# Optimization experiments

Hardware: AMD Instinct MI355X
Metric: run time of the kernel (lower is better)

## Reference

```python
import jax, jax.numpy as jnp
import numpy as np

B, N, C_IN, H, C_OUT = 8, 1024, 256, 4, 256
C = C_OUT // H  # per-head dim = 64
ALPHA = 0.2
NEG_INF = -9e15


def setup_inputs() -> dict:
    key = jax.random.key(0)
    k1, k2, k3, k4, k5 = jax.random.split(key, 5)
    node_feats = jax.random.normal(k1, (B, N, C_IN), dtype=jnp.float32)
    adj_matrix = jax.random.randint(k2, (B, N, N), 0, 2, dtype=jnp.int32)
    # include self-loops as GAT expects
    eye = jnp.eye(N, dtype=jnp.int32)[None]
    adj_matrix = jnp.maximum(adj_matrix, eye)
    # xavier_uniform with gain=1.414
    def xavier(k, shape, fan_in, fan_out, gain=1.414):
        lim = gain * np.sqrt(6.0 / (fan_in + fan_out))
        return jax.random.uniform(k, shape, jnp.float32, -lim, lim)
    W = xavier(k3, (C_OUT, C_IN), C_IN, C_OUT)          # projection weight [out,in]
    b = jnp.zeros((C_OUT,), dtype=jnp.float32)           # projection bias
    a = xavier(k4, (H, 2 * C), 2 * C, H)                 # attention vector per head
    return {"node_feats": node_feats, "adj_matrix": adj_matrix, "W": W, "b": b, "a": a}


def reference(node_feats, adj_matrix, W, b, a):
    Bb, Nn, _ = node_feats.shape
    Hh, twoC = a.shape
    Cc = twoC // 2
    # linear projection -> [B, N, H, C]
    h = (node_feats @ W.T + b).reshape(Bb, Nn, Hh, Cc)
    # edge logit(i,j) = leakyrelu(a . [h_i, h_j]) = leakyrelu(a1.h_i + a2.h_j)
    a_src, a_dst = a[:, :Cc], a[:, Cc:]
    l_src = jnp.einsum('bihc,hc->bih', h, a_src)  # [B,N,H]
    l_dst = jnp.einsum('bjhc,hc->bjh', h, a_dst)  # [B,N,H]
    logits = jax.nn.leaky_relu(l_src[:, :, None, :] + l_dst[:, None, :, :], ALPHA)  # [B,N,N,H]
    logits = jnp.where(adj_matrix[..., None] == 1, logits, NEG_INF)
    probs = jax.nn.softmax(logits, axis=2)  # softmax over neighbors j
    out = jnp.einsum('bijh,bjhc->bihc', probs, h)  # aggregate
    return out.reshape(Bb, Nn, Hh * Cc)  # concat heads
```

## Files before the change

kernel.cpp:

```cpp
#include <hip/hip_runtime.h>
#include <hip/hip_bf16.h>

#define BN   8
#define NN   1024
#define CIN  256
#define COUT 256
#define HH   4
#define CC   64
#define ALPHA_C 0.2f

typedef __attribute__((ext_vector_type(8))) short short8;
typedef __attribute__((ext_vector_type(4))) float f32x4;

__device__ __forceinline__ unsigned short f2bf(float x) {
    __hip_bfloat16 h = __float2bfloat16(x);
    return *(unsigned short*)&h;
}
__device__ __forceinline__ float bf2f(unsigned short u) {
    return __uint_as_float(((unsigned int)u) << 16);
}

__global__ __launch_bounds__(256) void k0_wpack(
    const float* __restrict__ W, unsigned short* __restrict__ Whp, unsigned short* __restrict__ Wlp)
{
    const int bid = blockIdx.x;
    const int n = threadIdx.x;
    const int fi = n * 64 + (bid >> 2) * 8 + (bid & 3) * 2;
    const float4* W4 = (const float4*)W;
    float4 wa = W4[fi], wb = W4[fi + 1];
    float xs[8] = {wa.x, wa.y, wa.z, wa.w, wb.x, wb.y, wb.z, wb.w};
    unsigned short hh[8], ll[8];
    #pragma unroll
    for (int e = 0; e < 8; ++e) {
        hh[e] = f2bf(xs[e]);
        ll[e] = f2bf(xs[e] - bf2f(hh[e]));
    }
    *(uint4*)(Whp + ((size_t)bid * 256 + n) * 8) = *(uint4*)hh;
    *(uint4*)(Wlp + ((size_t)bid * 256 + n) * 8) = *(uint4*)ll;
}

__global__ __launch_bounds__(1024, 4) void k1_gemm(
    const float* __restrict__ X, const float* __restrict__ bias, const float* __restrict__ a,
    const unsigned short* __restrict__ Whp, const unsigned short* __restrict__ Wlp,
    unsigned short* __restrict__ hbf_p, float* __restrict__ lsrc_t, float* __restrict__ ldst_t)
{
    __shared__ __align__(16) unsigned short Xh[32 * 256];
    __shared__ __align__(16) unsigned short Xl[32 * 256];
    __shared__ float lsP[2][8][2][16];

    const int bid = blockIdx.x;
    const int row0 = bid * 32;
    const int b  = bid >> 5;
    const int tj = bid & 31;
    const int tid = threadIdx.x;
    const int wv = tid >> 6, l = tid & 63, il = l & 15, jg = l >> 4;
    const int mq = wv >> 3, no = wv & 7;

    {
        const float4* X4 = (const float4*)(X + (size_t)row0 * CIN);
        #pragma unroll
        for (int it = 0; it < 2; ++it) {
            int f = it * 1024 + tid;
            int r = f >> 6, k4 = f & 63;
            float4 x = X4[f];
            unsigned short h0 = f2bf(x.x), h1 = f2bf(x.y), h2 = f2bf(x.z), h3 = f2bf(x.w);
            unsigned short l0 = f2bf(x.x - bf2f(h0)), l1 = f2bf(x.y - bf2f(h1));
            unsigned short l2 = f2bf(x.z - bf2f(h2)), l3 = f2bf(x.w - bf2f(h3));
            unsigned short hs[4] = {h0, h1, h2, h3}, ls[4] = {l0, l1, l2, l3};
            int off = r * 512 + ((k4 * 8) ^ ((r & 7) << 4));
            *(uint2*)((char*)Xh + off) = *(uint2*)hs;
            *(uint2*)((char*)Xl + off) = *(uint2*)ls;
        }
    }
    __syncthreads();

    f32x4 acc0 = {0.f, 0.f, 0.f, 0.f}, acc1 = acc0;
    {
        const int abase = (mq * 16 + il) * 512;
        const int swz = (il & 7) << 4;
        const short8* Wh8 = (const short8*)Whp;
        const short8* Wl8 = (const short8*)Wlp;
        const int nb = no * 32 + il;
        #pragma unroll
        for (int kc = 0; kc < 8; ++kc) {
            const int ab = abase + ((kc * 64 + jg * 16) ^ swz);
            short8 Ah = *(const short8*)((const char*)Xh + ab);
            short8 Al = *(const short8*)((const char*)Xl + ab);
            const int pidx = (kc * 4 + jg) * 256 + nb;
            short8 Bh0 = Wh8[pidx],      Bl0 = Wl8[pidx];
            short8 Bh1 = Wh8[pidx + 16], Bl1 = Wl8[pidx + 16];
            acc0 = __builtin_amdgcn_mfma_f32_16x16x32_bf16(Ah, Bh0, acc0, 0, 0, 0);
            acc1 = __builtin_amdgcn_mfma_f32_16x16x32_bf16(Ah, Bh1, acc1, 0, 0, 0);
            acc0 = __builtin_amdgcn_mfma_f32_16x16x32_bf16(Ah, Bl0, acc0, 0, 0, 0);
            acc1 = __builtin_amdgcn_mfma_f32_16x16x32_bf16(Ah, Bl1, acc1, 0, 0, 0);
            acc0 = __builtin_amdgcn_mfma_f32_16x16x32_bf16(Al, Bh0, acc0, 0, 0, 0);
            acc1 = __builtin_amdgcn_mfma_f32_16x16x32_bf16(Al, Bh1, acc1, 0, 0, 0);
        }
    }

    const int c0 = no * 32 + il, c1 = c0 + 16;
    const float bia0 = bias[c0], bia1 = bias[c1];
    const int hh = no >> 1;
    const int cc0 = c0 & 63, cc1 = c1 & 63;
    const float as0 = a[hh * 128 + cc0],      as1 = a[hh * 128 + cc1];
    const float ad0 = a[hh * 128 + 64 + cc0], ad1 = a[hh * 128 + 64 + cc1];

    float v0[4], v1[4], psrc[4], pdst[4];
    #pragma unroll
    for (int r = 0; r < 4; ++r) {
        v0[r] = acc0[r] + bia0;
        v1[r] = acc1[r] + bia1;
        psrc[r] = v0[r] * as0 + v1[r] * as1;
        pdst[r] = v0[r] * ad0 + v1[r] * ad1;
    }
    #pragma unroll
    for (int off = 8; off >= 1; off >>= 1) {
        #pragma unroll
        for (int r = 0; r < 4; ++r) {
            psrc[r] += __shfl_xor(psrc[r], off);
            pdst[r] += __shfl_xor(pdst[r], off);
        }
    }
    __syncthreads();

    unsigned short* hp = Xh;
    #pragma unroll
    for (int r = 0; r < 4; ++r) {
        int m = mq * 16 + 4 * jg + r;
        int base = (m >> 3) * 128 + (m & 7);
        hp[(c0 >> 6) * 2048 + ((c0 & 63) >> 4) * 512 + base + (c0 & 15) * 8] = f2bf(v0[r]);
        hp[(c1 >> 6) * 2048 + ((c1 & 63) >> 4) * 512 + base + (c1 & 15) * 8] = f2bf(v1[r]);
    }
    if (il == 0) {
        #pragma unroll
        for (int r = 0; r < 4; ++r) {
            lsP[0][no][mq][4 * jg + r] = psrc[r];
            lsP[1][no][mq][4 * jg + r] = pdst[r];
        }
    }
    __syncthreads();

    {
        uint4* dst4 = (uint4*)(hbf_p + (size_t)(b * 32 + tj) * 8192);
        dst4[tid] = ((const uint4*)hp)[tid];
    }
    if (tid < 256) {
        int sd = tid >> 7, rem = tid & 127, h2 = rem >> 5, m = rem & 31;
        float v = lsP[sd][2 * h2][m >> 4][m & 15] + lsP[sd][2 * h2 + 1][m >> 4][m & 15];
        float* dst = sd ? ldst_t : lsrc_t;
        dst[((size_t)b * HH + h2) * NN + tj * 32 + m] = v;
    }
}

__global__ __launch_bounds__(1024, 4) void k2_attn(
    const unsigned short* __restrict__ hbf_p, const int* __restrict__ adj,
    const float* __restrict__ lsrc_t, const float* __restrict__ ldst_t,
    float* __restrict__ out)
{
    __shared__ __align__(16) char smem[65536];
    __shared__ float lsumS[2][4][32];

    unsigned int (*adjw)[32] = (unsigned int (*)[32])smem;
    float* ldsTbl = (float*)(smem + 4096);

    const int bid = blockIdx.x;
    const int b  = bid & 7;
    const int i0 = (bid >> 3) * 32;
    const int tid = threadIdx.x;
    const int wv = tid >> 6, l = tid & 63, il = l & 15, jg = l >> 4;
    const int h = wv & 3, mq = (wv >> 2) & 1, jh = wv >> 3;

    {
        const int* arow = adj + ((size_t)b * NN + i0 + 2 * wv) * NN;
        #pragma unroll
        for (int rr = 0; rr < 2; ++rr)
            #pragma unroll 4
            for (int it = 0; it < 16; ++it) {
                int av = arow[rr * NN + it * 64 + l];
                unsigned long long mb = __ballot(av != 0);
                if (l == 0) {
                    adjw[2 * it][2 * wv + rr] = (unsigned int)mb;
                    adjw[2 * it + 1][2 * wv + rr] = (unsigned int)(mb >> 32);
                }
            }
    }
    ((float4*)ldsTbl)[tid] = ((const float4*)(ldst_t + (size_t)b * HH * NN))[tid];

    const float lsrc_v = lsrc_t[((size_t)b * HH + h) * NN + i0 + mq * 16 + il];

    __syncthreads();

    float mx = -3.4e38f;
    #pragma unroll
    for (int jt = 0; jt < 16; ++jt) mx = fmaxf(mx, ldsTbl[h * 1024 + jt * 64 + l]);
    #pragma unroll
    for (int off = 32; off >= 1; off >>= 1) mx = fmaxf(mx, __shfl_xor(mx, off));
    const float t0 = lsrc_v + mx;
    const float m_r = fmaxf(t0, ALPHA_C * t0);
    float lsum = 0.f;

    f32x4 acc0 = {0.f,0.f,0.f,0.f}, acc1 = acc0, acc2 = acc0, acc3 = acc0;

    const short8* bfp = (const short8*)(hbf_p + (size_t)b * 32 * 8192);
    const int fb = h * 256 + l;

    int tj = jh;
    short8 c0 = bfp[tj * 1024 + fb +   0];
    short8 c1 = bfp[tj * 1024 + fb +  64];
    short8 c2 = bfp[tj * 1024 + fb + 128];
    short8 c3 = bfp[tj * 1024 + fb + 192];

    for (int r = 0; r < 16; ++r) {
        const int tjn = (r < 15) ? (2 * (r + 1) + jh) : tj;
        short8 n0 = bfp[tjn * 1024 + fb +   0];
        short8 n1 = bfp[tjn * 1024 + fb +  64];
        short8 n2 = bfp[tjn * 1024 + fb + 128];
        short8 n3 = bfp[tjn * 1024 + fb + 192];

        unsigned int bw = adjw[2 * r + jh][mq * 16 + il] >> (jg * 8);
        const float* lt = ldsTbl + h * 1024 + r * 64 + jh * 32 + jg * 8;
        float4 dA = *(const float4*)lt;
        float4 dB = *(const float4*)(lt + 4);
        short8 af;
        #define PELEM(DV, E) {                                   \
            float s = lsrc_v + (DV);                             \
            s = fmaxf(s, ALPHA_C * s);                           \
            float p = __expf(s - m_r);                           \
            p = (bw & (1u << (E))) ? p : 0.f;                    \
            lsum += p;                                           \
            af[E] = (short)f2bf(p); }
        PELEM(dA.x, 0) PELEM(dA.y, 1) PELEM(dA.z, 2) PELEM(dA.w, 3)
        PELEM(dB.x, 4) PELEM(dB.y, 5) PELEM(dB.z, 6) PELEM(dB.w, 7)
        #undef PELEM

        acc0 = __builtin_amdgcn_mfma_f32_16x16x32_bf16(af, c0, acc0, 0, 0, 0);
        acc1 = __builtin_amdgcn_mfma_f32_16x16x32_bf16(af, c1, acc1, 0, 0, 0);
        acc2 = __builtin_amdgcn_mfma_f32_16x16x32_bf16(af, c2, acc2, 0, 0, 0);
        acc3 = __builtin_amdgcn_mfma_f32_16x16x32_bf16(af, c3, acc3, 0, 0, 0);

        c0 = n0; c1 = n1; c2 = n2; c3 = n3;
        tj = tjn;
    }

    lsum += __shfl_xor(lsum, 16);
    lsum += __shfl_xor(lsum, 32);
    if (l < 16) lsumS[jh][h][mq * 16 + l] = lsum;
    __syncthreads();

    float* red = (float*)smem;
    {
        float* rw = red + wv * 1024;
        #pragma unroll
        for (int rr = 0; rr < 4; ++rr) {
            rw[(4 * jg + rr) * 64 +  0 + il] = acc0[rr];
            rw[(4 * jg + rr) * 64 + 16 + il] = acc1[rr];
            rw[(4 * jg + rr) * 64 + 32 + il] = acc2[rr];
            rw[(4 * jg + rr) * 64 + 48 + il] = acc3[rr];
        }
    }
    __syncthreads();

    #pragma unroll
    for (int e = 0; e < 8; ++e) {
        int flat = e * 1024 + tid;
        int m = flat >> 8, c = flat & 255;
        int h2 = c >> 6, mq2 = m >> 4, r16 = m & 15, cl = c & 63;
        float vA = red[(mq2 * 4 + h2) * 1024 + r16 * 64 + cl];
        float vB = red[(8 + mq2 * 4 + h2) * 1024 + r16 * 64 + cl];
        float ls = lsumS[0][h2][m] + lsumS[1][h2][m];
        out[((size_t)b * NN + i0 + m) * 256 + c] = (vA + vB) / ls;
    }
}

extern "C" void kernel_launch(void* const* d_in, const int* in_sizes, int n_in,
                              void* d_out, int out_size, void* d_ws, size_t ws_size,
                              hipStream_t stream) {
    const float* X    = (const float*)d_in[0];
    const int*   adj  = (const int*)  d_in[1];
    const float* W    = (const float*)d_in[2];
    const float* bias = (const float*)d_in[3];
    const float* a    = (const float*)d_in[4];
    float* out = (float*)d_out;

    unsigned short* hbf_p = (unsigned short*)d_ws;
    float* lsrc_t = (float*)(hbf_p + (size_t)BN * 32 * 8192);
    float* ldst_t = lsrc_t + (size_t)BN * HH * NN;
    unsigned short* Whp = (unsigned short*)(ldst_t + (size_t)BN * HH * NN);
    unsigned short* Wlp = Whp + 65536;

    k0_wpack<<<32, 256, 0, stream>>>(W, Whp, Wlp);
    k1_gemm<<<256, 1024, 0, stream>>>(X, bias, a, Whp, Wlp, hbf_p, lsrc_t, ldst_t);
    k2_attn<<<256, 1024, 0, stream>>>(hbf_p, adj, lsrc_t, ldst_t, out);
}
```

Baseline: 48.13 us.

## Reuse B fragments across both row halves and split neighbors four ways per head

```diff
diff --git a/kernel.cpp b/kernel.cpp
--- a/kernel.cpp
+++ b/kernel.cpp
@@ -157,8 +157,8 @@
     const float* __restrict__ lsrc_t, const float* __restrict__ ldst_t,
     float* __restrict__ out)
 {
-    __shared__ __align__(16) char smem[65536];
-    __shared__ float lsumS[2][4][32];
+    __shared__ __align__(16) char smem[32768];
+    __shared__ float lsumS[4][4][32];
 
     unsigned int (*adjw)[32] = (unsigned int (*)[32])smem;
     float* ldsTbl = (float*)(smem + 4096);
@@ -168,13 +168,13 @@
     const int i0 = (bid >> 3) * 32;
     const int tid = threadIdx.x;
     const int wv = tid >> 6, l = tid & 63, il = l & 15, jg = l >> 4;
-    const int h = wv & 3, mq = (wv >> 2) & 1, jh = wv >> 3;
+    const int h = wv & 3, jh = wv >> 2;
 
     {
         const int* arow = adj + ((size_t)b * NN + i0 + 2 * wv) * NN;
         #pragma unroll
         for (int rr = 0; rr < 2; ++rr)
-            #pragma unroll 4
+            #pragma unroll
             for (int it = 0; it < 16; ++it) {
                 int av = arow[rr * NN + it * 64 + l];
                 unsigned long long mb = __ballot(av != 0);
@@ -186,7 +186,8 @@
     }
     ((float4*)ldsTbl)[tid] = ((const float4*)(ldst_t + (size_t)b * HH * NN))[tid];
 
-    const float lsrc_v = lsrc_t[((size_t)b * HH + h) * NN + i0 + mq * 16 + il];
+    const float lsrc_v0 = lsrc_t[((size_t)b * HH + h) * NN + i0 + il];
+    const float lsrc_v1 = lsrc_t[((size_t)b * HH + h) * NN + i0 + 16 + il];
 
     __syncthreads();
 
@@ -195,80 +196,114 @@
     for (int jt = 0; jt < 16; ++jt) mx = fmaxf(mx, ldsTbl[h * 1024 + jt * 64 + l]);
     #pragma unroll
     for (int off = 32; off >= 1; off >>= 1) mx = fmaxf(mx, __shfl_xor(mx, off));
-    const float t0 = lsrc_v + mx;
-    const float m_r = fmaxf(t0, ALPHA_C * t0);
-    float lsum = 0.f;
-
-    f32x4 acc0 = {0.f,0.f,0.f,0.f}, acc1 = acc0, acc2 = acc0, acc3 = acc0;
+    const float t00 = lsrc_v0 + mx;
+    const float t01 = lsrc_v1 + mx;
+    const float m_r0 = fmaxf(t00, ALPHA_C * t00);
+    const float m_r1 = fmaxf(t01, ALPHA_C * t01);
+    float lsA0 = 0.f, lsA1 = 0.f, lsB0 = 0.f, lsB1 = 0.f;
+
+    f32x4 acc00 = {0.f,0.f,0.f,0.f}, acc01 = acc00, acc02 = acc00, acc03 = acc00;
+    f32x4 acc10 = acc00, acc11 = acc00, acc12 = acc00, acc13 = acc00;
 
     const short8* bfp = (const short8*)(hbf_p + (size_t)b * 32 * 8192);
     const int fb = h * 256 + l;
 
-    int tj = jh;
-    short8 c0 = bfp[tj * 1024 + fb +   0];
-    short8 c1 = bfp[tj * 1024 + fb +  64];
-    short8 c2 = bfp[tj * 1024 + fb + 128];
-    short8 c3 = bfp[tj * 1024 + fb + 192];
-
-    for (int r = 0; r < 16; ++r) {
-        const int tjn = (r < 15) ? (2 * (r + 1) + jh) : tj;
-        short8 n0 = bfp[tjn * 1024 + fb +   0];
-        short8 n1 = bfp[tjn * 1024 + fb +  64];
-        short8 n2 = bfp[tjn * 1024 + fb + 128];
-        short8 n3 = bfp[tjn * 1024 + fb + 192];
-
-        unsigned int bw = adjw[2 * r + jh][mq * 16 + il] >> (jg * 8);
-        const float* lt = ldsTbl + h * 1024 + r * 64 + jh * 32 + jg * 8;
-        float4 dA = *(const float4*)lt;
-        float4 dB = *(const float4*)(lt + 4);
-        short8 af;
-        #define PELEM(DV, E) {                                   \
-            float s = lsrc_v + (DV);                             \
-            s = fmaxf(s, ALPHA_C * s);                           \
-            float p = __expf(s - m_r);                           \
-            p = (bw & (1u << (E))) ? p : 0.f;                    \
-            lsum += p;                                           \
-            af[E] = (short)f2bf(p); }
-        PELEM(dA.x, 0) PELEM(dA.y, 1) PELEM(dA.z, 2) PELEM(dA.w, 3)
-        PELEM(dB.x, 4) PELEM(dB.y, 5) PELEM(dB.z, 6) PELEM(dB.w, 7)
-        #undef PELEM
-
-        acc0 = __builtin_amdgcn_mfma_f32_16x16x32_bf16(af, c0, acc0, 0, 0, 0);
-        acc1 = __builtin_amdgcn_mfma_f32_16x16x32_bf16(af, c1, acc1, 0, 0, 0);
-        acc2 = __builtin_amdgcn_mfma_f32_16x16x32_bf16(af, c2, acc2, 0, 0, 0);
-        acc3 = __builtin_amdgcn_mfma_f32_16x16x32_bf16(af, c3, acc3, 0, 0, 0);
-
-        c0 = n0; c1 = n1; c2 = n2; c3 = n3;
-        tj = tjn;
-    }
-
-    lsum += __shfl_xor(lsum, 16);
-    lsum += __shfl_xor(lsum, 32);
-    if (l < 16) lsumS[jh][h][mq * 16 + l] = lsum;
+    short8 A0, A1, A2, A3, B0, B1, B2, B3;
+    #define LD(P, RND) { const int t_ = 4 * (RND) + jh;               \
+        P##0 = bfp[t_ * 1024 + fb +   0];                             \
+        P##1 = bfp[t_ * 1024 + fb +  64];                             \
+        P##2 = bfp[t_ * 1024 + fb + 128];                             \
+        P##3 = bfp[t_ * 1024 + fb + 192]; }
+
+    #define PEL(AF, E, DV, BW, LSV, MR, LS) {                         \
+        float s_ = (LSV) + (DV); s_ = fmaxf(s_, ALPHA_C * s_);        \
+        float p_ = __expf(s_ - (MR));                                 \
+        p_ = ((BW >> (E)) & 1u) ? p_ : 0.f;                           \
+        LS += p_; AF[E] = (short)f2bf(p_); }
+
+    #define ROUND(P, RND) {                                           \
+        const int tj_ = 4 * (RND) + jh;                               \
+        const unsigned int bw0 = adjw[tj_][il] >> (jg * 8);           \
+        const unsigned int bw1 = adjw[tj_][16 + il] >> (jg * 8);      \
+        const float* lt_ = ldsTbl + h * 1024 + tj_ * 32 + jg * 8;     \
+        const float4 dA = *(const float4*)lt_;                        \
+        const float4 dB = *(const float4*)(lt_ + 4);                  \
+        short8 af0, af1;                                              \
+        PEL(af0, 0, dA.x, bw0, lsrc_v0, m_r0, lsA0)                   \
+        PEL(af0, 1, dA.y, bw0, lsrc_v0, m_r0, lsA0)                   \
+        PEL(af0, 2, dA.z, bw0, lsrc_v0, m_r0, lsA0)                   \
+        PEL(af0, 3, dA.w, bw0, lsrc_v0, m_r0, lsA0)                   \
+        PEL(af0, 4, dB.x, bw0, lsrc_v0, m_r0, lsA1)                   \
+        PEL(af0, 5, dB.y, bw0, lsrc_v0, m_r0, lsA1)                   \
+        PEL(af0, 6, dB.z, bw0, lsrc_v0, m_r0, lsA1)                   \
+        PEL(af0, 7, dB.w, bw0, lsrc_v0, m_r0, lsA1)                   \
+        PEL(af1, 0, dA.x, bw1, lsrc_v1, m_r1, lsB0)                   \
+        PEL(af1, 1, dA.y, bw1, lsrc_v1, m_r1, lsB0)                   \
+        PEL(af1, 2, dA.z, bw1, lsrc_v1, m_r1, lsB0)                   \
+        PEL(af1, 3, dA.w, bw1, lsrc_v1, m_r1, lsB0)                   \
+        PEL(af1, 4, dB.x, bw1, lsrc_v1, m_r1, lsB1)                   \
+        PEL(af1, 5, dB.y, bw1, lsrc_v1, m_r1, lsB1)                   \
+        PEL(af1, 6, dB.z, bw1, lsrc_v1, m_r1, lsB1)                   \
+        PEL(af1, 7, dB.w, bw1, lsrc_v1, m_r1, lsB1)                   \
+        acc00 = __builtin_amdgcn_mfma_f32_16x16x32_bf16(af0, P##0, acc00, 0, 0, 0); \
+        acc01 = __builtin_amdgcn_mfma_f32_16x16x32_bf16(af0, P##1, acc01, 0, 0, 0); \
+        acc02 = __builtin_amdgcn_mfma_f32_16x16x32_bf16(af0, P##2, acc02, 0, 0, 0); \
+        acc03 = __builtin_amdgcn_mfma_f32_16x16x32_bf16(af0, P##3, acc03, 0, 0, 0); \
+        acc10 = __builtin_amdgcn_mfma_f32_16x16x32_bf16(af1, P##0, acc10, 0, 0, 0); \
+        acc11 = __builtin_amdgcn_mfma_f32_16x16x32_bf16(af1, P##1, acc11, 0, 0, 0); \
+        acc12 = __builtin_amdgcn_mfma_f32_16x16x32_bf16(af1, P##2, acc12, 0, 0, 0); \
+        acc13 = __builtin_amdgcn_mfma_f32_16x16x32_bf16(af1, P##3, acc13, 0, 0, 0); }
+
+    LD(A, 0)
+    LD(B, 1)
+    for (int rr = 0; rr < 4; ++rr) {
+        ROUND(A, 2 * rr)
+        if (rr < 3) LD(A, 2 * rr + 2)
+        ROUND(B, 2 * rr + 1)
+        if (rr < 3) LD(B, 2 * rr + 3)
+    }
+    #undef LD
+    #undef PEL
+    #undef ROUND
+
+    float ls0 = lsA0 + lsA1, ls1 = lsB0 + lsB1;
+    ls0 += __shfl_xor(ls0, 16); ls0 += __shfl_xor(ls0, 32);
+    ls1 += __shfl_xor(ls1, 16); ls1 += __shfl_xor(ls1, 32);
+    if (l < 16) {
+        lsumS[jh][h][l] = ls0;
+        lsumS[jh][h][16 + l] = ls1;
+    }
     __syncthreads();
 
     float* red = (float*)smem;
-    {
-        float* rw = red + wv * 1024;
-        #pragma unroll
-        for (int rr = 0; rr < 4; ++rr) {
-            rw[(4 * jg + rr) * 64 +  0 + il] = acc0[rr];
-            rw[(4 * jg + rr) * 64 + 16 + il] = acc1[rr];
-            rw[(4 * jg + rr) * 64 + 32 + il] = acc2[rr];
-            rw[(4 * jg + rr) * 64 + 48 + il] = acc3[rr];
-        }
-    }
-    __syncthreads();
+    #define STORE1(ACC, MQ, S, OP) {                                              \
+        red[((MQ)*16 + 4*jg + 0) * 256 + h * 64 + (S)*16 + il] OP ACC[0];         \
+        red[((MQ)*16 + 4*jg + 1) * 256 + h * 64 + (S)*16 + il] OP ACC[1];         \
+        red[((MQ)*16 + 4*jg + 2) * 256 + h * 64 + (S)*16 + il] OP ACC[2];         \
+        red[((MQ)*16 + 4*jg + 3) * 256 + h * 64 + (S)*16 + il] OP ACC[3]; }
+    #define STOREALL(OP) {                                                        \
+        STORE1(acc00, 0, 0, OP) STORE1(acc01, 0, 1, OP)                           \
+        STORE1(acc02, 0, 2, OP) STORE1(acc03, 0, 3, OP)                           \
+        STORE1(acc10, 1, 0, OP) STORE1(acc11, 1, 1, OP)                           \
+        STORE1(acc12, 1, 2, OP) STORE1(acc13, 1, 3, OP) }
+    if (jh == 0) STOREALL(=)
+    __syncthreads();
+    if (jh == 1) STOREALL(+=)
+    __syncthreads();
+    if (jh == 2) STOREALL(+=)
+    __syncthreads();
+    if (jh == 3) STOREALL(+=)
+    __syncthreads();
+    #undef STORE1
+    #undef STOREALL
 
     #pragma unroll
     for (int e = 0; e < 8; ++e) {
         int flat = e * 1024 + tid;
         int m = flat >> 8, c = flat & 255;
-        int h2 = c >> 6, mq2 = m >> 4, r16 = m & 15, cl = c & 63;
-        float vA = red[(mq2 * 4 + h2) * 1024 + r16 * 64 + cl];
-        float vB = red[(8 + mq2 * 4 + h2) * 1024 + r16 * 64 + cl];
-        float ls = lsumS[0][h2][m] + lsumS[1][h2][m];
-        out[((size_t)b * NN + i0 + m) * 256 + c] = (vA + vB) / ls;
+        int h2 = c >> 6;
+        float ls = lsumS[0][h2][m] + lsumS[1][h2][m] + lsumS[2][h2][m] + lsumS[3][h2][m];
+        out[((size_t)b * NN + i0 + m) * 256 + c] = red[m * 256 + c] / ls;
     }
 }
 
```

New measurement: 52.07 us. +8.2%, slower.

## Shrink attention blocks to 16 rows with full j-loop per wave

Applied to the files above, without the earlier changes.

```diff
diff --git a/kernel.cpp b/kernel.cpp
--- a/kernel.cpp
+++ b/kernel.cpp
@@ -39,7 +39,7 @@
     *(uint4*)(Wlp + ((size_t)bid * 256 + n) * 8) = *(uint4*)ll;
 }
 
-__global__ __launch_bounds__(1024, 4) void k1_gemm(
+__global__ __launch_bounds__(1024, 1) void k1_gemm(
     const float* __restrict__ X, const float* __restrict__ bias, const float* __restrict__ a,
     const unsigned short* __restrict__ Whp, const unsigned short* __restrict__ Wlp,
     unsigned short* __restrict__ hbf_p, float* __restrict__ lsrc_t, float* __restrict__ ldst_t)
@@ -152,41 +152,43 @@
     }
 }
 
-__global__ __launch_bounds__(1024, 4) void k2_attn(
+__global__ __launch_bounds__(256, 2) void k2_attn(
     const unsigned short* __restrict__ hbf_p, const int* __restrict__ adj,
     const float* __restrict__ lsrc_t, const float* __restrict__ ldst_t,
     float* __restrict__ out)
 {
-    __shared__ __align__(16) char smem[65536];
-    __shared__ float lsumS[2][4][32];
-
-    unsigned int (*adjw)[32] = (unsigned int (*)[32])smem;
-    float* ldsTbl = (float*)(smem + 4096);
+    __shared__ unsigned int adjw[32][16];
+    __shared__ float ldsTbl[4 * 1024];
 
     const int bid = blockIdx.x;
     const int b  = bid & 7;
-    const int i0 = (bid >> 3) * 32;
+    const int i0 = (bid >> 3) * 16;
     const int tid = threadIdx.x;
-    const int wv = tid >> 6, l = tid & 63, il = l & 15, jg = l >> 4;
-    const int h = wv & 3, mq = (wv >> 2) & 1, jh = wv >> 3;
-
-    {
-        const int* arow = adj + ((size_t)b * NN + i0 + 2 * wv) * NN;
-        #pragma unroll
-        for (int rr = 0; rr < 2; ++rr)
-            #pragma unroll 4
+    const int h  = tid >> 6;
+    const int l  = tid & 63, il = l & 15, jg = l >> 4;
+
+    {
+        const int* arow = adj + ((size_t)b * NN + i0 + 4 * h) * NN;
+        #pragma unroll
+        for (int rr = 0; rr < 4; ++rr) {
+            #pragma unroll
             for (int it = 0; it < 16; ++it) {
                 int av = arow[rr * NN + it * 64 + l];
                 unsigned long long mb = __ballot(av != 0);
                 if (l == 0) {
-                    adjw[2 * it][2 * wv + rr] = (unsigned int)mb;
-                    adjw[2 * it + 1][2 * wv + rr] = (unsigned int)(mb >> 32);
+                    adjw[2 * it    ][4 * h + rr] = (unsigned int)mb;
+                    adjw[2 * it + 1][4 * h + rr] = (unsigned int)(mb >> 32);
                 }
             }
-    }
-    ((float4*)ldsTbl)[tid] = ((const float4*)(ldst_t + (size_t)b * HH * NN))[tid];
-
-    const float lsrc_v = lsrc_t[((size_t)b * HH + h) * NN + i0 + mq * 16 + il];
+        }
+    }
+    {
+        const float4* src = (const float4*)(ldst_t + (size_t)b * HH * NN);
+        #pragma unroll
+        for (int k = 0; k < 4; ++k)
+            ((float4*)ldsTbl)[k * 256 + tid] = src[k * 256 + tid];
+    }
+    const float lsrc_v = lsrc_t[((size_t)b * HH + h) * NN + i0 + il];
 
     __syncthreads();
 
@@ -195,7 +197,7 @@
     for (int jt = 0; jt < 16; ++jt) mx = fmaxf(mx, ldsTbl[h * 1024 + jt * 64 + l]);
     #pragma unroll
     for (int off = 32; off >= 1; off >>= 1) mx = fmaxf(mx, __shfl_xor(mx, off));
-    const float t0 = lsrc_v + mx;
+    const float t0  = lsrc_v + mx;
     const float m_r = fmaxf(t0, ALPHA_C * t0);
     float lsum = 0.f;
 
@@ -204,31 +206,31 @@
     const short8* bfp = (const short8*)(hbf_p + (size_t)b * 32 * 8192);
     const int fb = h * 256 + l;
 
-    int tj = jh;
-    short8 c0 = bfp[tj * 1024 + fb +   0];
-    short8 c1 = bfp[tj * 1024 + fb +  64];
-    short8 c2 = bfp[tj * 1024 + fb + 128];
-    short8 c3 = bfp[tj * 1024 + fb + 192];
-
-    for (int r = 0; r < 16; ++r) {
-        const int tjn = (r < 15) ? (2 * (r + 1) + jh) : tj;
-        short8 n0 = bfp[tjn * 1024 + fb +   0];
-        short8 n1 = bfp[tjn * 1024 + fb +  64];
-        short8 n2 = bfp[tjn * 1024 + fb + 128];
-        short8 n3 = bfp[tjn * 1024 + fb + 192];
-
-        unsigned int bw = adjw[2 * r + jh][mq * 16 + il] >> (jg * 8);
-        const float* lt = ldsTbl + h * 1024 + r * 64 + jh * 32 + jg * 8;
-        float4 dA = *(const float4*)lt;
-        float4 dB = *(const float4*)(lt + 4);
+    short8 c0 = bfp[fb +   0];
+    short8 c1 = bfp[fb +  64];
+    short8 c2 = bfp[fb + 128];
+    short8 c3 = bfp[fb + 192];
+
+    #pragma unroll 2
+    for (int t = 0; t < 32; ++t) {
+        const int tn = (t < 31) ? t + 1 : 31;
+        short8 n0 = bfp[tn * 1024 + fb +   0];
+        short8 n1 = bfp[tn * 1024 + fb +  64];
+        short8 n2 = bfp[tn * 1024 + fb + 128];
+        short8 n3 = bfp[tn * 1024 + fb + 192];
+
+        const unsigned int bw = adjw[t][il] >> (jg * 8);
+        const float* lt = ldsTbl + h * 1024 + t * 32 + jg * 8;
+        const float4 dA = *(const float4*)lt;
+        const float4 dB = *(const float4*)(lt + 4);
         short8 af;
         #define PELEM(DV, E) {                                   \
-            float s = lsrc_v + (DV);                             \
-            s = fmaxf(s, ALPHA_C * s);                           \
-            float p = __expf(s - m_r);                           \
-            p = (bw & (1u << (E))) ? p : 0.f;                    \
-            lsum += p;                                           \
-            af[E] = (short)f2bf(p); }
+            float s_ = lsrc_v + (DV);                            \
+            s_ = fmaxf(s_, ALPHA_C * s_);                        \
+            float p_ = __expf(s_ - m_r);                         \
+            p_ = ((bw >> (E)) & 1u) ? p_ : 0.f;                  \
+            lsum += p_;                                          \
+            af[E] = (short)f2bf(p_); }
         PELEM(dA.x, 0) PELEM(dA.y, 1) PELEM(dA.z, 2) PELEM(dA.w, 3)
         PELEM(dB.x, 4) PELEM(dB.y, 5) PELEM(dB.z, 6) PELEM(dB.w, 7)
         #undef PELEM
@@ -239,36 +241,23 @@
         acc3 = __builtin_amdgcn_mfma_f32_16x16x32_bf16(af, c3, acc3, 0, 0, 0);
 
         c0 = n0; c1 = n1; c2 = n2; c3 = n3;
-        tj = tjn;
     }
 
     lsum += __shfl_xor(lsum, 16);
     lsum += __shfl_xor(lsum, 32);
-    if (l < 16) lsumS[jh][h][mq * 16 + l] = lsum;
-    __syncthreads();
-
-    float* red = (float*)smem;
-    {
-        float* rw = red + wv * 1024;
-        #pragma unroll
-        for (int rr = 0; rr < 4; ++rr) {
-            rw[(4 * jg + rr) * 64 +  0 + il] = acc0[rr];
-            rw[(4 * jg + rr) * 64 + 16 + il] = acc1[rr];
-            rw[(4 * jg + rr) * 64 + 32 + il] = acc2[rr];
-            rw[(4 * jg + rr) * 64 + 48 + il] = acc3[rr];
-        }
-    }
-    __syncthreads();
-
-    #pragma unroll
-    for (int e = 0; e < 8; ++e) {
-        int flat = e * 1024 + tid;
-        int m = flat >> 8, c = flat & 255;
-        int h2 = c >> 6, mq2 = m >> 4, r16 = m & 15, cl = c & 63;
-        float vA = red[(mq2 * 4 + h2) * 1024 + r16 * 64 + cl];
-        float vB = red[(8 + mq2 * 4 + h2) * 1024 + r16 * 64 + cl];
-        float ls = lsumS[0][h2][m] + lsumS[1][h2][m];
-        out[((size_t)b * NN + i0 + m) * 256 + c] = (vA + vB) / ls;
+
+    float inv[4];
+    #pragma unroll
+    for (int r = 0; r < 4; ++r) inv[r] = 1.0f / __shfl(lsum, 4 * jg + r);
+
+    float* outp = out + ((size_t)b * NN + i0) * COUT + h * 64 + il;
+    #pragma unroll
+    for (int r = 0; r < 4; ++r) {
+        const size_t ro = (size_t)(4 * jg + r) * COUT;
+        outp[ro +  0] = acc0[r] * inv[r];
+        outp[ro + 16] = acc1[r] * inv[r];
+        outp[ro + 32] = acc2[r] * inv[r];
+        outp[ro + 48] = acc3[r] * inv[r];
     }
 }
 
@@ -290,5 +279,5 @@
 
     k0_wpack<<<32, 256, 0, stream>>>(W, Whp, Wlp);
     k1_gemm<<<256, 1024, 0, stream>>>(X, bias, a, Whp, Wlp, hbf_p, lsrc_t, ldst_t);
-    k2_attn<<<256, 1024, 0, stream>>>(hbf_p, adj, lsrc_t, ldst_t, out);
-}
+    k2_attn<<<BN * (NN / 16), 256, 0, stream>>>(hbf_p, adj, lsrc_t, ldst_t, out);
+}
```

Result: slower. 61.06 us (+26.9%).
